# Kernel optimization log

Hardware: AMD Instinct MI355X
Metric: run time of the kernel (lower is better)

## Reference

```python
import jax, jax.numpy as jnp
import numpy as np

N_NODES = 100000
N_EDGES = 1600000
D = 128
N_GRAPHS = 8


def setup_inputs() -> dict:
    key = jax.random.key(0)
    ks = jax.random.split(key, 10)
    x = jax.random.normal(ks[0], (N_NODES, D), dtype=jnp.float32)
    src = jax.random.randint(ks[1], (N_EDGES,), 0, N_NODES)
    dst = jax.random.randint(ks[2], (N_EDGES,), 0, N_NODES)
    graph_ids = jnp.sort(jax.random.randint(ks[3], (N_NODES,), 0, N_GRAPHS))
    s = 1.0 / np.sqrt(D)
    W1 = jax.random.normal(ks[4], (D, D), dtype=jnp.float32) * s
    b1 = jnp.zeros((D,), dtype=jnp.float32)
    W2 = jax.random.normal(ks[5], (D, D), dtype=jnp.float32) * s
    b2 = jnp.zeros((D,), dtype=jnp.float32)
    prelu_a = jnp.full((1,), 0.25, dtype=jnp.float32)
    lin_W = jax.random.normal(ks[6], (D, 1), dtype=jnp.float32) * s
    lin_b = jnp.zeros((1,), dtype=jnp.float32)
    return {"x": x, "src": src, "dst": dst, "graph_ids": graph_ids,
            "W1": W1, "b1": b1, "W2": W2, "b2": b2,
            "prelu_a": prelu_a, "lin_W": lin_W, "lin_b": lin_b}


def _gcn_layer(h, src, dst, n_src, n_dst, W, b):
    # GraphConv with symmetric ('both') normalization: D^{-1/2} A D^{-1/2} H W + b
    h = h @ W                                      # [N, D] small GEMM
    m = h[src] * n_src[:, None]                    # [E, D] gather (irregular)
    agg = jax.ops.segment_sum(m, dst, num_segments=N_NODES)  # scatter-add
    return agg * n_dst[:, None] + b


def reference(x, src, dst, graph_ids, W1, b1, W2, b2, prelu_a, lin_W, lin_b):
    ones_e = jnp.ones((src.shape[0],), dtype=x.dtype)
    deg_out = jnp.maximum(jax.ops.segment_sum(ones_e, src, num_segments=N_NODES), 1.0)
    deg_in = jnp.maximum(jax.ops.segment_sum(ones_e, dst, num_segments=N_NODES), 1.0)
    n_src = jax.lax.rsqrt(deg_out)[src]            # per-edge source norm
    n_dst = jax.lax.rsqrt(deg_in)                  # per-node dest norm

    h = _gcn_layer(x, src, dst, n_src, n_dst, W1, b1)
    h = jax.nn.relu(h)
    h = _gcn_layer(h, src, dst, n_src, n_dst, W2, b2)
    h = jax.nn.relu(h)

    # dgl.mean_nodes: per-graph mean over nodes
    sums = jax.ops.segment_sum(h, graph_ids, num_segments=N_GRAPHS)   # [G, D]
    cnt = jax.ops.segment_sum(jnp.ones((N_NODES,), h.dtype), graph_ids,
                              num_segments=N_GRAPHS)
    pooled = sums / jnp.maximum(cnt, 1.0)[:, None]

    # PReLU (single shared slope) -> Linear -> Sigmoid
    pooled = jnp.where(pooled > 0, pooled, prelu_a[0] * pooled)
    out = jax.nn.sigmoid(pooled @ lin_W + lin_b)   # [G, 1]
    return out
```

## Files before the change

### kernel.cpp

```cpp
#include <hip/hip_runtime.h>
#include <hip/hip_bf16.h>

#define NN 100000
#define NE 1600000
#define DD 128
#define NG 8

#define BSH 8
#define KB 391
#define BMASK 255
#define PB 512
#define CHUNK 3125
#define SCAN_N (KB * PB)

typedef unsigned short u16;
typedef unsigned char u8;
typedef __attribute__((ext_vector_type(8))) short short8;
typedef __attribute__((ext_vector_type(4))) float f32x4;
typedef __attribute__((ext_vector_type(2))) float f32x2;

static __device__ __forceinline__ float bf2f(u16 u) {
  return __uint_as_float(((unsigned)u) << 16);
}
static __device__ __forceinline__ u16 f2bf(float f) {
  unsigned u = __float_as_uint(f);
  u += 0x7fffu + ((u >> 16) & 1);
  return (u16)(u >> 16);
}
static __device__ __forceinline__ u8 f2fp8(float f) {
  return (u8)(__builtin_amdgcn_cvt_pk_fp8_f32(f, f, 0, false) & 0xFF);
}

__global__ void fill_zero(float* __restrict__ p, int n4) {
  int i = blockIdx.x * blockDim.x + threadIdx.x;
  if (i < n4) ((float4*)p)[i] = make_float4(0.f, 0.f, 0.f, 0.f);
}

__global__ void conv_xscale(const float* __restrict__ in, const float* __restrict__ rs_out,
                            u8* __restrict__ out, int n8) {
  int i = blockIdx.x * blockDim.x + threadIdx.x;
  if (i >= n8) return;
  float w = rs_out[i >> 4];
  const float4* p = (const float4*)(in + (size_t)i * 8);
  float4 a = p[0], b = p[1];
  int lo = 0, hi = 0;
  lo = __builtin_amdgcn_cvt_pk_fp8_f32(a.x * w, a.y * w, lo, false);
  lo = __builtin_amdgcn_cvt_pk_fp8_f32(a.z * w, a.w * w, lo, true);
  hi = __builtin_amdgcn_cvt_pk_fp8_f32(b.x * w, b.y * w, hi, false);
  hi = __builtin_amdgcn_cvt_pk_fp8_f32(b.z * w, b.w * w, hi, true);
  ((uint2*)out)[i] = make_uint2((unsigned)lo, (unsigned)hi);
}

__global__ void conv_w_transpose(const float* __restrict__ W, u16* __restrict__ Wt) {
  int idx = blockIdx.x * blockDim.x + threadIdx.x;
  if (idx >= DD * DD) return;
  int n = idx >> 7, k = idx & 127;
  Wt[idx] = f2bf(W[k * DD + n]);
}

__global__ __launch_bounds__(256) void histo_gid(const int* __restrict__ gid,
                                                 int* __restrict__ cnt) {
  __shared__ int h[NG];
  int t = threadIdx.x;
  if (t < NG) h[t] = 0;
  __syncthreads();
  for (int i = blockIdx.x * 256 + t; i < NN; i += gridDim.x * 256)
    atomicAdd(&h[gid[i]], 1);
  __syncthreads();
  if (t < NG && h[t]) atomicAdd(&cnt[t], h[t]);
}

__global__ __launch_bounds__(256) void p1_both(const int* __restrict__ src,
                                               const int* __restrict__ dst,
                                               int* __restrict__ countsS,
                                               int* __restrict__ countsD) {
  __shared__ int hs[KB], hd[KB];
  int t = threadIdx.x, blk = blockIdx.x;
  for (int i = t; i < KB; i += 256) { hs[i] = 0; hd[i] = 0; }
  __syncthreads();
  int e0 = blk * CHUNK;
  for (int i = t; i < CHUNK; i += 256) {
    atomicAdd(&hs[src[e0 + i] >> BSH], 1);
    atomicAdd(&hd[dst[e0 + i] >> BSH], 1);
  }
  __syncthreads();
  for (int i = t; i < KB; i += 256) {
    countsS[i * PB + blk] = hs[i];
    countsD[i * PB + blk] = hd[i];
  }
}

__global__ __launch_bounds__(256) void scanA(int* __restrict__ countsS,
                                             int* __restrict__ countsD,
                                             int* __restrict__ totS,
                                             int* __restrict__ totD) {
  __shared__ int data[PB];
  __shared__ int part[256];
  int b = blockIdx.x;
  int isS = (b < KB);
  int k = isS ? b : b - KB;
  int* counts = isS ? countsS : countsD;
  int* tot = isS ? totS : totD;
  int t = threadIdx.x;
  int* c = counts + (size_t)k * PB;
  data[t] = c[t];
  data[t + 256] = c[t + 256];
  __syncthreads();
  int a0 = data[2 * t], a1 = data[2 * t + 1];
  int s = a0 + a1;
  part[t] = s;
  __syncthreads();
  for (int off = 1; off < 256; off <<= 1) {
    int v = (t >= off) ? part[t - off] : 0;
    __syncthreads();
    part[t] += v;
    __syncthreads();
  }
  int ex = part[t] - s;
  data[2 * t] = ex;
  data[2 * t + 1] = ex + a0;
  __syncthreads();
  c[t] = data[t];
  c[t + 256] = data[t + 256];
  if (t == 255) tot[k] = part[255];
}

__global__ __launch_bounds__(256) void scanB(const int* __restrict__ totS,
                                             const int* __restrict__ totD,
                                             int* __restrict__ baseS,
                                             int* __restrict__ baseD) {
  __shared__ int data[512];
  __shared__ int part[256];
  const int* tot = blockIdx.x ? totD : totS;
  int* base = blockIdx.x ? baseD : baseS;
  int t = threadIdx.x;
  data[t] = (t < KB) ? tot[t] : 0;
  data[t + 256] = (t + 256 < KB) ? tot[t + 256] : 0;
  __syncthreads();
  int a0 = data[2 * t], a1 = data[2 * t + 1];
  int s = a0 + a1;
  part[t] = s;
  __syncthreads();
  for (int off = 1; off < 256; off <<= 1) {
    int v = (t >= off) ? part[t - off] : 0;
    __syncthreads();
    part[t] += v;
    __syncthreads();
  }
  int ex = part[t] - s;
  int i0 = 2 * t, i1 = 2 * t + 1;
  if (i0 <= KB) base[i0] = ex;
  if (i1 <= KB) base[i1] = ex + a0;
}

__global__ __launch_bounds__(256) void p2_both(const int* __restrict__ src,
                                               const int* __restrict__ dst,
                                               const int* __restrict__ countsS,
                                               const int* __restrict__ countsD,
                                               const int* __restrict__ baseS,
                                               const int* __restrict__ baseD,
                                               u8* __restrict__ recsS,
                                               unsigned* __restrict__ recsD) {
  __shared__ int curS[KB], curD[KB];
  int t = threadIdx.x, blk = blockIdx.x;
  for (int i = t; i < KB; i += 256) {
    curS[i] = countsS[i * PB + blk] + baseS[i];
    curD[i] = countsD[i * PB + blk] + baseD[i];
  }
  __syncthreads();
  int e0 = blk * CHUNK;
  for (int i = t; i < CHUNK; i += 256) {
    int s = src[e0 + i];
    int d = dst[e0 + i];
    int ps = atomicAdd(&curS[s >> BSH], 1);
    recsS[ps] = (u8)(s & BMASK);
    int pd = atomicAdd(&curD[d >> BSH], 1);
    recsD[pd] = (unsigned)s | ((unsigned)(d & BMASK) << 17);
  }
}

__global__ __launch_bounds__(256) void src_p3(const u8* __restrict__ recsS,
                                              const int* __restrict__ baseS,
                                              float* __restrict__ rs_out) {
  __shared__ int hist[256];
  int k = blockIdx.x, t = threadIdx.x;
  int rbeg = baseS[k];
  int rend = baseS[k + 1];
  hist[t] = 0;
  __syncthreads();
  for (int i = rbeg + t; i < rend; i += 256) atomicAdd(&hist[recsS[i]], 1);
  __syncthreads();
  int n = (k << BSH) + t;
  if (n < NN) rs_out[n] = rsqrtf(fmaxf((float)hist[t], 1.f));
}

__global__ __launch_bounds__(256) void csr_p3(const unsigned* __restrict__ recs,
                                              const int* __restrict__ baseD,
                                              int* __restrict__ csr_src,
                                              int* __restrict__ cursor_end,
                                              int* __restrict__ deg_in,
                                              float* __restrict__ rs_in) {
  __shared__ int hist[256];
  __shared__ int part[256];
  int k = blockIdx.x, t = threadIdx.x;
  int rbeg = baseD[k];
  int rend = baseD[k + 1];
  hist[t] = 0;
  __syncthreads();
  for (int i = rbeg + t; i < rend; i += 256) atomicAdd(&hist[recs[i] >> 17], 1);
  __syncthreads();
  int h = hist[t];
  part[t] = h;
  __syncthreads();
  for (int off = 1; off < 256; off <<= 1) {
    int v = (t >= off) ? part[t - off] : 0;
    __syncthreads();
    part[t] += v;
    __syncthreads();
  }
  int run = rbeg + part[t] - h;
  int n = (k << BSH) + t;
  if (n < NN) {
    cursor_end[n] = run + h;
    deg_in[n] = h;
    rs_in[n] = rsqrtf(fmaxf((float)h, 1.f));
  }
  hist[t] = run;
  __syncthreads();
  for (int i = rbeg + t; i < rend; i += 256) {
    unsigned r = recs[i];
    int pos = atomicAdd(&hist[r >> 17], 1);
    csr_src[pos] = (int)(r & 0x1FFFF);
  }
}

__global__ __launch_bounds__(256) void gather_agg_fp8(
    const uint4* __restrict__ Hv, const int* __restrict__ csr_src,
    const int* __restrict__ cursor_end, const int* __restrict__ deg_in,
    u16* __restrict__ agg) {
  int node = blockIdx.x * 32 + (threadIdx.x >> 3);
  if (node >= NN) return;
  int q = threadIdx.x & 7;
  int end = cursor_end[node];
  int j = end - deg_in[node];
  float acc[16];
#pragma unroll
  for (int i = 0; i < 16; ++i) acc[i] = 0.f;
#define ACCV(v) { f32x2 t_;                                                        \
  t_ = __builtin_amdgcn_cvt_pk_f32_fp8((int)(v).x, false); acc[0] += t_.x;  acc[1] += t_.y;  \
  t_ = __builtin_amdgcn_cvt_pk_f32_fp8((int)(v).x, true);  acc[2] += t_.x;  acc[3] += t_.y;  \
  t_ = __builtin_amdgcn_cvt_pk_f32_fp8((int)(v).y, false); acc[4] += t_.x;  acc[5] += t_.y;  \
  t_ = __builtin_amdgcn_cvt_pk_f32_fp8((int)(v).y, true);  acc[6] += t_.x;  acc[7] += t_.y;  \
  t_ = __builtin_amdgcn_cvt_pk_f32_fp8((int)(v).z, false); acc[8] += t_.x;  acc[9] += t_.y;  \
  t_ = __builtin_amdgcn_cvt_pk_f32_fp8((int)(v).z, true);  acc[10] += t_.x; acc[11] += t_.y; \
  t_ = __builtin_amdgcn_cvt_pk_f32_fp8((int)(v).w, false); acc[12] += t_.x; acc[13] += t_.y; \
  t_ = __builtin_amdgcn_cvt_pk_f32_fp8((int)(v).w, true);  acc[14] += t_.x; acc[15] += t_.y; }
  for (; j + 4 <= end; j += 4) {
    int s0 = csr_src[j + 0];
    int s1 = csr_src[j + 1];
    int s2 = csr_src[j + 2];
    int s3 = csr_src[j + 3];
    uint4 v0 = Hv[(size_t)s0 * 8 + q];
    uint4 v1 = Hv[(size_t)s1 * 8 + q];
    uint4 v2 = Hv[(size_t)s2 * 8 + q];
    uint4 v3 = Hv[(size_t)s3 * 8 + q];
    ACCV(v0) ACCV(v1) ACCV(v2) ACCV(v3)
  }
  for (; j < end; ++j) {
    uint4 v = Hv[(size_t)csr_src[j] * 8 + q];
    ACCV(v)
  }
#undef ACCV
  uint4 o0, o1;
  o0.x = (unsigned)f2bf(acc[0])  | ((unsigned)f2bf(acc[1])  << 16);
  o0.y = (unsigned)f2bf(acc[2])  | ((unsigned)f2bf(acc[3])  << 16);
  o0.z = (unsigned)f2bf(acc[4])  | ((unsigned)f2bf(acc[5])  << 16);
  o0.w = (unsigned)f2bf(acc[6])  | ((unsigned)f2bf(acc[7])  << 16);
  o1.x = (unsigned)f2bf(acc[8])  | ((unsigned)f2bf(acc[9])  << 16);
  o1.y = (unsigned)f2bf(acc[10]) | ((unsigned)f2bf(acc[11]) << 16);
  o1.z = (unsigned)f2bf(acc[12]) | ((unsigned)f2bf(acc[13]) << 16);
  o1.w = (unsigned)f2bf(acc[14]) | ((unsigned)f2bf(acc[15]) << 16);
  u16* op = agg + (size_t)node * DD + q * 16;
  *(uint4*)op = o0;
  *(uint4*)(op + 8) = o1;
}

#define GEMM_PRE                                                              \
  __shared__ uint4 Wl4[2048];                                      \
  int tid = threadIdx.x;                                                      \
  {                                                                           \
    const uint4* Wg4 = (const uint4*)Wt;                                      \
    for (int i = tid; i < 2048; i += 256) {                                   \
      int row = i >> 4, c = i & 15;                                           \
      Wl4[(row << 4) | (c ^ (row & 15))] = Wg4[i];                            \
    }                                                                         \
  }                                                                           \
  int wid = tid >> 6;                                                         \
  int lane = tid & 63;                                                        \
  int l15 = lane & 15;                                                        \
  int kg = lane >> 4;                                                         \
  int rowbase = blockIdx.x * 128 + wid * 32;                                  \
  f32x4 acc[2][8];                                                            \
  short8 a[2][4];                                                             \
  _Pragma("unroll")                                                           \
  for (int t = 0; t < 2; ++t) {                                               \
    int arow = rowbase + t * 16 + l15;                                        \
    bool ok = arow < NN;                                                      \
    const u16* aptr = Ab + (size_t)arow * DD + kg * 8;                        \
    _Pragma("unroll")                                                         \
    for (int kt = 0; kt < 4; ++kt) {                                          \
      a[t][kt] = ok ? *(const short8*)(aptr + kt * 32)                        \
                    : (short8){0, 0, 0, 0, 0, 0, 0, 0};                       \
      acc[0][kt] = (f32x4){0.f, 0.f, 0.f, 0.f};                               \
      acc[0][kt + 4] = (f32x4){0.f, 0.f, 0.f, 0.f};                           \
      acc[1][kt] = (f32x4){0.f, 0.f, 0.f, 0.f};                               \
      acc[1][kt + 4] = (f32x4){0.f, 0.f, 0.f, 0.f};                           \
    }                                                                         \
  }                                                                           \
  __syncthreads();                                                            \
  _Pragma("unroll")                                                           \
  for (int n = 0; n < 8; ++n) {                                               \
    _Pragma("unroll")                                                         \
    for (int kt = 0; kt < 4; ++kt) {                                          \
      short8 b = *(const short8*)(Wl4 + (((n * 16 + l15) << 4) |              \
                                         ((kg + kt * 4) ^ l15)));             \
      acc[0][n] = __builtin_amdgcn_mfma_f32_16x16x32_bf16(a[0][kt], b, acc[0][n], 0, 0, 0); \
      acc[1][n] = __builtin_amdgcn_mfma_f32_16x16x32_bf16(a[1][kt], b, acc[1][n], 0, 0, 0); \
    }                                                                         \
  }

__global__ __launch_bounds__(256) void gemm_mfma_fp8out(
    const u16* __restrict__ Ab, const u16* __restrict__ Wt,
    const float* __restrict__ bias, const float* __restrict__ rs,
    const float* __restrict__ post, u8* __restrict__ Cb) {
  GEMM_PRE
#pragma unroll
  for (int t = 0; t < 2; ++t) {
    int crow0 = rowbase + t * 16 + kg * 4;
#pragma unroll
    for (int j = 0; j < 4; ++j) {
      int r = crow0 + j;
      if (r < NN) {
        float s = rs[r];
        float ps = post[r];
#pragma unroll
        for (int n = 0; n < 8; ++n) {
          float v = fmaxf(acc[t][n][j] * s + bias[n * 16 + l15], 0.f) * ps;
          Cb[(size_t)r * DD + n * 16 + l15] = f2fp8(v);
        }
      }
    }
  }
}

__global__ __launch_bounds__(256) void gemm_mfma_pool(
    const u16* __restrict__ Ab, const u16* __restrict__ Wt,
    const float* __restrict__ bias, const float* __restrict__ rs,
    const int* __restrict__ gid, float* __restrict__ pooled) {
  __shared__ float pl[NG * DD];
  for (int i = threadIdx.x; i < NG * DD; i += 256) pl[i] = 0.f;
  GEMM_PRE
  float pacc[8];
#pragma unroll
  for (int n = 0; n < 8; ++n) pacc[n] = 0.f;
  int curg = -1;
#pragma unroll
  for (int t = 0; t < 2; ++t) {
    int crow0 = rowbase + t * 16 + kg * 4;
#pragma unroll
    for (int j = 0; j < 4; ++j) {
      int r = crow0 + j;
      if (r < NN) {
        int g = gid[r];
        if (g != curg) {
          if (curg >= 0) {
#pragma unroll
            for (int n = 0; n < 8; ++n) {
              atomicAdd(&pl[curg * DD + n * 16 + l15], pacc[n]);
              pacc[n] = 0.f;
            }
          }
          curg = g;
        }
        float s = rs[r];
#pragma unroll
        for (int n = 0; n < 8; ++n)
          pacc[n] += fmaxf(acc[t][n][j] * s + bias[n * 16 + l15], 0.f);
      }
    }
  }
  if (curg >= 0) {
#pragma unroll
    for (int n = 0; n < 8; ++n)
      atomicAdd(&pl[curg * DD + n * 16 + l15], pacc[n]);
  }
  __syncthreads();
  int rlo = blockIdx.x * 128;
  int rhi = rlo + 127;
  if (rhi >= NN) rhi = NN - 1;
  int gmin = gid[rlo];
  int gmax = gid[rhi];
  int span = (gmax - gmin + 1) * DD;
  for (int i = tid; i < span; i += 256) {
    float v = pl[gmin * DD + i];
    if (v != 0.f) atomicAdd(&pooled[gmin * DD + i], v);
  }
}

__global__ __launch_bounds__(128) void final_kernel(const float* __restrict__ pooled,
                                                    const int* __restrict__ cnt,
                                                    const float* __restrict__ prelu_a,
                                                    const float* __restrict__ linW,
                                                    const float* __restrict__ linb,
                                                    float* __restrict__ out) {
  int t = threadIdx.x;
  __shared__ float red[2];
  float w = linW[t];
  float alpha = prelu_a[0];
  float lb = linb[0];
  for (int g = 0; g < NG; ++g) {
    float v = pooled[g * DD + t] / fmaxf((float)cnt[g], 1.f);
    v = v > 0.f ? v : alpha * v;
    float p = v * w;
#pragma unroll
    for (int off = 32; off >= 1; off >>= 1) p += __shfl_down(p, off, 64);
    if ((t & 63) == 0) red[t >> 6] = p;
    __syncthreads();
    if (t == 0) {
      float s = red[0] + red[1] + lb;
      out[g] = 1.f / (1.f + expf(-s));
    }
    __syncthreads();
  }
}

extern "C" void kernel_launch(void* const* d_in, const int* in_sizes, int n_in,
                              void* d_out, int out_size, void* d_ws, size_t ws_size,
                              hipStream_t stream) {
  const float* x   = (const float*)d_in[0];
  const int*   src = (const int*)d_in[1];
  const int*   dst = (const int*)d_in[2];
  const int*   gid = (const int*)d_in[3];
  const float* W1  = (const float*)d_in[4];
  const float* b1  = (const float*)d_in[5];
  const float* W2  = (const float*)d_in[6];
  const float* b2  = (const float*)d_in[7];
  const float* pa  = (const float*)d_in[8];
  const float* lW  = (const float*)d_in[9];
  const float* lb  = (const float*)d_in[10];
  float* out = (float*)d_out;

  char* ws = (char*)d_ws;
  size_t o = 0;
  auto alloc = [&](size_t bytes) {
    size_t r = o;
    o += (bytes + 255) & ~(size_t)255;
    return r;
  };
  int*   deg_in  = (int*)(ws + alloc((size_t)NN * 4));
  float* rs_out  = (float*)(ws + alloc((size_t)NN * 4));
  float* rs_in   = (float*)(ws + alloc((size_t)NN * 4));
  int*   countsS = (int*)(ws + alloc((size_t)SCAN_N * 4));
  int*   countsD = (int*)(ws + alloc((size_t)SCAN_N * 4));
  int*   totS    = (int*)(ws + alloc((size_t)KB * 4));
  int*   totD    = (int*)(ws + alloc((size_t)KB * 4));
  int*   baseS   = (int*)(ws + alloc((size_t)(KB + 1) * 4));
  int*   baseD   = (int*)(ws + alloc((size_t)(KB + 1) * 4));
  int*   cursor_end = (int*)(ws + alloc((size_t)NN * 4));
  u8*    recsS   = (u8*)(ws + alloc((size_t)NE));
  unsigned* recsD = (unsigned*)(ws + alloc((size_t)NE * 4));
  int*   csr_src = (int*)(ws + alloc((size_t)NE * 4));
  u16*   Wt1     = (u16*)(ws + alloc((size_t)DD * DD * 2));
  u16*   Wt2     = (u16*)(ws + alloc((size_t)DD * DD * 2));
  u8*    bufA    = (u8*)(ws + alloc((size_t)NN * DD));
  u8*    bufB    = (u8*)(ws + alloc((size_t)NN * DD));
  u16*   aggbuf  = (u16*)(ws + alloc((size_t)NN * DD * 2));
  float* pooled  = (float*)(ws + alloc((size_t)(NG * DD + NG) * 4));
  int*   cnt     = (int*)(pooled + NG * DD);

  fill_zero<<<2, 256, 0, stream>>>(pooled, (NG * DD + NG + 3) / 4);
  histo_gid<<<98, 256, 0, stream>>>(gid, cnt);

  p1_both<<<PB, 256, 0, stream>>>(src, dst, countsS, countsD);
  scanA<<<2 * KB, 256, 0, stream>>>(countsS, countsD, totS, totD);
  scanB<<<2, 256, 0, stream>>>(totS, totD, baseS, baseD);
  p2_both<<<PB, 256, 0, stream>>>(src, dst, countsS, countsD, baseS, baseD, recsS, recsD);
  src_p3<<<KB, 256, 0, stream>>>(recsS, baseS, rs_out);
  csr_p3<<<KB, 256, 0, stream>>>(recsD, baseD, csr_src, cursor_end, deg_in, rs_in);

  conv_xscale<<<(NN * DD / 8 + 255) / 256, 256, 0, stream>>>(x, rs_out, bufA, NN * DD / 8);
  conv_w_transpose<<<64, 256, 0, stream>>>(W1, Wt1);
  conv_w_transpose<<<64, 256, 0, stream>>>(W2, Wt2);

  const int gablocks = (NN + 31) / 32;
  const int gmblocks = (NN + 127) / 128;

  gather_agg_fp8<<<gablocks, 256, 0, stream>>>((const uint4*)bufA, csr_src, cursor_end, deg_in, aggbuf);
  gemm_mfma_fp8out<<<gmblocks, 256, 0, stream>>>(aggbuf, Wt1, b1, rs_in, rs_out, bufB);

  gather_agg_fp8<<<gablocks, 256, 0, stream>>>((const uint4*)bufB, csr_src, cursor_end, deg_in, aggbuf);
  gemm_mfma_pool<<<gmblocks, 256, 0, stream>>>(aggbuf, Wt2, b2, rs_in, gid, pooled);

  final_kernel<<<1, 128, 0, stream>>>(pooled, cnt, pa, lW, lb, out);
}
```

Measured before the change: 212.3 us.

## Slice fp8 features into column-major slices for gather, fuse preprocessing kernels

Stores the fp8 node features as 8 slices of 16 bytes per node, so each gather block handles one slice for 256 nodes. Each slice (1.6 MB) is small enough to stay cached during the random gathers. It also merges the W transposes, graph-id histogram and pooled zeroing into the first histogram kernel, and merges the source and destination degree/CSR passes into one launch, which cuts launch count. The trade-off is that each edge index is now read eight times (once per slice) and each thread loads one 16-byte value per edge instead of eight lanes sharing a 128-byte row.

```diff
diff --git a/kernel.cpp b/kernel.cpp
--- a/kernel.cpp
+++ b/kernel.cpp
@@ -12,6 +12,8 @@
 #define PB 512
 #define CHUNK 3125
 #define SCAN_N (KB * PB)
+#define NSL 8
+#define GHB 98
 
 typedef unsigned short u16;
 typedef unsigned char u8;
@@ -31,16 +33,12 @@
   return (u8)(__builtin_amdgcn_cvt_pk_fp8_f32(f, f, 0, false) & 0xFF);
 }
 
-__global__ void fill_zero(float* __restrict__ p, int n4) {
-  int i = blockIdx.x * blockDim.x + threadIdx.x;
-  if (i < n4) ((float4*)p)[i] = make_float4(0.f, 0.f, 0.f, 0.f);
-}
-
 __global__ void conv_xscale(const float* __restrict__ in, const float* __restrict__ rs_out,
                             u8* __restrict__ out, int n8) {
   int i = blockIdx.x * blockDim.x + threadIdx.x;
   if (i >= n8) return;
-  float w = rs_out[i >> 4];
+  int node = i >> 4, c = i & 15;
+  float w = rs_out[node];
   const float4* p = (const float4*)(in + (size_t)i * 8);
   float4 a = p[0], b = p[1];
   int lo = 0, hi = 0;
@@ -48,45 +46,57 @@
   lo = __builtin_amdgcn_cvt_pk_fp8_f32(a.z * w, a.w * w, lo, true);
   hi = __builtin_amdgcn_cvt_pk_fp8_f32(b.x * w, b.y * w, hi, false);
   hi = __builtin_amdgcn_cvt_pk_fp8_f32(b.z * w, b.w * w, hi, true);
-  ((uint2*)out)[i] = make_uint2((unsigned)lo, (unsigned)hi);
-}
-
-__global__ void conv_w_transpose(const float* __restrict__ W, u16* __restrict__ Wt) {
-  int idx = blockIdx.x * blockDim.x + threadIdx.x;
-  if (idx >= DD * DD) return;
-  int n = idx >> 7, k = idx & 127;
-  Wt[idx] = f2bf(W[k * DD + n]);
-}
-
-__global__ __launch_bounds__(256) void histo_gid(const int* __restrict__ gid,
-                                                 int* __restrict__ cnt) {
-  __shared__ int h[NG];
-  int t = threadIdx.x;
-  if (t < NG) h[t] = 0;
-  __syncthreads();
-  for (int i = blockIdx.x * 256 + t; i < NN; i += gridDim.x * 256)
-    atomicAdd(&h[gid[i]], 1);
-  __syncthreads();
-  if (t < NG && h[t]) atomicAdd(&cnt[t], h[t]);
-}
-
-__global__ __launch_bounds__(256) void p1_both(const int* __restrict__ src,
-                                               const int* __restrict__ dst,
-                                               int* __restrict__ countsS,
-                                               int* __restrict__ countsD) {
+  *(uint2*)(out + ((size_t)(c >> 1) * NN + node) * 16 + (c & 1) * 8) =
+      make_uint2((unsigned)lo, (unsigned)hi);
+}
+
+__global__ __launch_bounds__(256) void p1x(const int* __restrict__ src,
+                                           const int* __restrict__ dst,
+                                           int* __restrict__ countsS,
+                                           int* __restrict__ countsD,
+                                           const float* __restrict__ W1,
+                                           const float* __restrict__ W2,
+                                           u16* __restrict__ Wt1,
+                                           u16* __restrict__ Wt2,
+                                           const int* __restrict__ gid,
+                                           int* __restrict__ cnt_part,
+                                           float* __restrict__ pooled) {
   __shared__ int hs[KB], hd[KB];
-  int t = threadIdx.x, blk = blockIdx.x;
-  for (int i = t; i < KB; i += 256) { hs[i] = 0; hd[i] = 0; }
-  __syncthreads();
-  int e0 = blk * CHUNK;
-  for (int i = t; i < CHUNK; i += 256) {
-    atomicAdd(&hs[src[e0 + i] >> BSH], 1);
-    atomicAdd(&hd[dst[e0 + i] >> BSH], 1);
-  }
-  __syncthreads();
-  for (int i = t; i < KB; i += 256) {
-    countsS[i * PB + blk] = hs[i];
-    countsD[i * PB + blk] = hd[i];
+  __shared__ int h8[NG];
+  int t = threadIdx.x, b = blockIdx.x;
+  if (b < PB) {
+    for (int i = t; i < KB; i += 256) { hs[i] = 0; hd[i] = 0; }
+    __syncthreads();
+    int e0 = b * CHUNK;
+    for (int i = t; i < CHUNK; i += 256) {
+      atomicAdd(&hs[src[e0 + i] >> BSH], 1);
+      atomicAdd(&hd[dst[e0 + i] >> BSH], 1);
+    }
+    __syncthreads();
+    for (int i = t; i < KB; i += 256) {
+      countsS[i * PB + b] = hs[i];
+      countsD[i * PB + b] = hd[i];
+    }
+  } else if (b < PB + 128) {
+    int i = (b - PB) * 256 + t;
+    if (i < DD * DD) {
+      int n = i >> 7, k = i & 127;
+      Wt1[i] = f2bf(W1[k * DD + n]);
+    } else {
+      int i2 = i - DD * DD;
+      int n = i2 >> 7, k = i2 & 127;
+      Wt2[i2] = f2bf(W2[k * DD + n]);
+    }
+  } else if (b < PB + 128 + GHB) {
+    int blk = b - PB - 128;
+    if (t < NG) h8[t] = 0;
+    __syncthreads();
+    for (int i = blk * 256 + t; i < NN; i += GHB * 256)
+      atomicAdd(&h8[gid[i]], 1);
+    __syncthreads();
+    if (t < NG) cnt_part[blk * NG + t] = h8[t];
+  } else {
+    for (int i = t; i < NG * DD; i += 256) pooled[i] = 0.f;
   }
 }
 
@@ -179,68 +189,70 @@
   }
 }
 
-__global__ __launch_bounds__(256) void src_p3(const u8* __restrict__ recsS,
-                                              const int* __restrict__ baseS,
-                                              float* __restrict__ rs_out) {
-  __shared__ int hist[256];
-  int k = blockIdx.x, t = threadIdx.x;
-  int rbeg = baseS[k];
-  int rend = baseS[k + 1];
-  hist[t] = 0;
-  __syncthreads();
-  for (int i = rbeg + t; i < rend; i += 256) atomicAdd(&hist[recsS[i]], 1);
-  __syncthreads();
-  int n = (k << BSH) + t;
-  if (n < NN) rs_out[n] = rsqrtf(fmaxf((float)hist[t], 1.f));
-}
-
-__global__ __launch_bounds__(256) void csr_p3(const unsigned* __restrict__ recs,
-                                              const int* __restrict__ baseD,
-                                              int* __restrict__ csr_src,
-                                              int* __restrict__ cursor_end,
-                                              int* __restrict__ deg_in,
-                                              float* __restrict__ rs_in) {
+__global__ __launch_bounds__(256) void sd_p3(const u8* __restrict__ recsS,
+                                             const int* __restrict__ baseS,
+                                             float* __restrict__ rs_out,
+                                             const unsigned* __restrict__ recsD,
+                                             const int* __restrict__ baseD,
+                                             int* __restrict__ csr_src,
+                                             int* __restrict__ cursor_end,
+                                             int* __restrict__ deg_in,
+                                             float* __restrict__ rs_in) {
   __shared__ int hist[256];
   __shared__ int part[256];
-  int k = blockIdx.x, t = threadIdx.x;
-  int rbeg = baseD[k];
-  int rend = baseD[k + 1];
-  hist[t] = 0;
-  __syncthreads();
-  for (int i = rbeg + t; i < rend; i += 256) atomicAdd(&hist[recs[i] >> 17], 1);
-  __syncthreads();
-  int h = hist[t];
-  part[t] = h;
-  __syncthreads();
-  for (int off = 1; off < 256; off <<= 1) {
-    int v = (t >= off) ? part[t - off] : 0;
-    __syncthreads();
-    part[t] += v;
-    __syncthreads();
-  }
-  int run = rbeg + part[t] - h;
-  int n = (k << BSH) + t;
-  if (n < NN) {
-    cursor_end[n] = run + h;
-    deg_in[n] = h;
-    rs_in[n] = rsqrtf(fmaxf((float)h, 1.f));
-  }
-  hist[t] = run;
-  __syncthreads();
-  for (int i = rbeg + t; i < rend; i += 256) {
-    unsigned r = recs[i];
-    int pos = atomicAdd(&hist[r >> 17], 1);
-    csr_src[pos] = (int)(r & 0x1FFFF);
-  }
-}
-
-__global__ __launch_bounds__(256) void gather_agg_fp8(
-    const uint4* __restrict__ Hv, const int* __restrict__ csr_src,
+  int t = threadIdx.x;
+  if (blockIdx.x < KB) {
+    int k = blockIdx.x;
+    int rbeg = baseS[k];
+    int rend = baseS[k + 1];
+    hist[t] = 0;
+    __syncthreads();
+    for (int i = rbeg + t; i < rend; i += 256) atomicAdd(&hist[recsS[i]], 1);
+    __syncthreads();
+    int n = (k << BSH) + t;
+    if (n < NN) rs_out[n] = rsqrtf(fmaxf((float)hist[t], 1.f));
+  } else {
+    int k = blockIdx.x - KB;
+    int rbeg = baseD[k];
+    int rend = baseD[k + 1];
+    hist[t] = 0;
+    __syncthreads();
+    for (int i = rbeg + t; i < rend; i += 256) atomicAdd(&hist[recsD[i] >> 17], 1);
+    __syncthreads();
+    int h = hist[t];
+    part[t] = h;
+    __syncthreads();
+    for (int off = 1; off < 256; off <<= 1) {
+      int v = (t >= off) ? part[t - off] : 0;
+      __syncthreads();
+      part[t] += v;
+      __syncthreads();
+    }
+    int run = rbeg + part[t] - h;
+    int n = (k << BSH) + t;
+    if (n < NN) {
+      cursor_end[n] = run + h;
+      deg_in[n] = h;
+      rs_in[n] = rsqrtf(fmaxf((float)h, 1.f));
+    }
+    hist[t] = run;
+    __syncthreads();
+    for (int i = rbeg + t; i < rend; i += 256) {
+      unsigned r = recsD[i];
+      int pos = atomicAdd(&hist[r >> 17], 1);
+      csr_src[pos] = (int)(r & 0x1FFFF);
+    }
+  }
+}
+
+__global__ __launch_bounds__(256) void gather_slice(
+    const uint4* __restrict__ Hs, const int* __restrict__ csr_src,
     const int* __restrict__ cursor_end, const int* __restrict__ deg_in,
     u16* __restrict__ agg) {
-  int node = blockIdx.x * 32 + (threadIdx.x >> 3);
+  int slice = blockIdx.x & (NSL - 1);
+  int node = (blockIdx.x >> 3) * 256 + threadIdx.x;
   if (node >= NN) return;
-  int q = threadIdx.x & 7;
+  const uint4* H = Hs + (size_t)slice * NN;
   int end = cursor_end[node];
   int j = end - deg_in[node];
   float acc[16];
@@ -260,14 +272,14 @@
     int s1 = csr_src[j + 1];
     int s2 = csr_src[j + 2];
     int s3 = csr_src[j + 3];
-    uint4 v0 = Hv[(size_t)s0 * 8 + q];
-    uint4 v1 = Hv[(size_t)s1 * 8 + q];
-    uint4 v2 = Hv[(size_t)s2 * 8 + q];
-    uint4 v3 = Hv[(size_t)s3 * 8 + q];
+    uint4 v0 = H[s0];
+    uint4 v1 = H[s1];
+    uint4 v2 = H[s2];
+    uint4 v3 = H[s3];
     ACCV(v0) ACCV(v1) ACCV(v2) ACCV(v3)
   }
   for (; j < end; ++j) {
-    uint4 v = Hv[(size_t)csr_src[j] * 8 + q];
+    uint4 v = H[csr_src[j]];
     ACCV(v)
   }
 #undef ACCV
@@ -280,7 +292,7 @@
   o1.y = (unsigned)f2bf(acc[10]) | ((unsigned)f2bf(acc[11]) << 16);
   o1.z = (unsigned)f2bf(acc[12]) | ((unsigned)f2bf(acc[13]) << 16);
   o1.w = (unsigned)f2bf(acc[14]) | ((unsigned)f2bf(acc[15]) << 16);
-  u16* op = agg + (size_t)node * DD + q * 16;
+  u16* op = agg + (size_t)node * DD + slice * 16;
   *(uint4*)op = o0;
   *(uint4*)(op + 8) = o1;
 }
@@ -346,7 +358,7 @@
 #pragma unroll
         for (int n = 0; n < 8; ++n) {
           float v = fmaxf(acc[t][n][j] * s + bias[n * 16 + l15], 0.f) * ps;
-          Cb[(size_t)r * DD + n * 16 + l15] = f2fp8(v);
+          Cb[((size_t)n * NN + r) * 16 + l15] = f2fp8(v);
         }
       }
     }
@@ -408,18 +420,25 @@
 }
 
 __global__ __launch_bounds__(128) void final_kernel(const float* __restrict__ pooled,
-                                                    const int* __restrict__ cnt,
+                                                    const int* __restrict__ cnt_part,
                                                     const float* __restrict__ prelu_a,
                                                     const float* __restrict__ linW,
                                                     const float* __restrict__ linb,
                                                     float* __restrict__ out) {
   int t = threadIdx.x;
   __shared__ float red[2];
+  __shared__ int cntl[NG];
+  if (t < NG) {
+    int s = 0;
+    for (int b = 0; b < GHB; ++b) s += cnt_part[b * NG + t];
+    cntl[t] = s;
+  }
+  __syncthreads();
   float w = linW[t];
   float alpha = prelu_a[0];
   float lb = linb[0];
   for (int g = 0; g < NG; ++g) {
-    float v = pooled[g * DD + t] / fmaxf((float)cnt[g], 1.f);
+    float v = pooled[g * DD + t] / fmaxf((float)cntl[g], 1.f);
     v = v > 0.f ? v : alpha * v;
     float p = v * w;
 #pragma unroll
@@ -475,31 +494,24 @@
   u8*    bufA    = (u8*)(ws + alloc((size_t)NN * DD));
   u8*    bufB    = (u8*)(ws + alloc((size_t)NN * DD));
   u16*   aggbuf  = (u16*)(ws + alloc((size_t)NN * DD * 2));
-  float* pooled  = (float*)(ws + alloc((size_t)(NG * DD + NG) * 4));
-  int*   cnt     = (int*)(pooled + NG * DD);
-
-  fill_zero<<<2, 256, 0, stream>>>(pooled, (NG * DD + NG + 3) / 4);
-  histo_gid<<<98, 256, 0, stream>>>(gid, cnt);
-
-  p1_both<<<PB, 256, 0, stream>>>(src, dst, countsS, countsD);
+  float* pooled  = (float*)(ws + alloc((size_t)NG * DD * 4));
+  int*   cnt_part = (int*)(ws + alloc((size_t)GHB * NG * 4));
+
+  p1x<<<PB + 128 + GHB + 1, 256, 0, stream>>>(src, dst, countsS, countsD,
+                                              W1, W2, Wt1, Wt2, gid, cnt_part, pooled);
   scanA<<<2 * KB, 256, 0, stream>>>(countsS, countsD, totS, totD);
   scanB<<<2, 256, 0, stream>>>(totS, totD, baseS, baseD);
   p2_both<<<PB, 256, 0, stream>>>(src, dst, countsS, countsD, baseS, baseD, recsS, recsD);
-  src_p3<<<KB, 256, 0, stream>>>(recsS, baseS, rs_out);
-  csr_p3<<<KB, 256, 0, stream>>>(recsD, baseD, csr_src, cursor_end, deg_in, rs_in);
-
+  sd_p3<<<2 * KB, 256, 0, stream>>>(recsS, baseS, rs_out,
+                                    recsD, baseD, csr_src, cursor_end, deg_in, rs_in);
   conv_xscale<<<(NN * DD / 8 + 255) / 256, 256, 0, stream>>>(x, rs_out, bufA, NN * DD / 8);
-  conv_w_transpose<<<64, 256, 0, stream>>>(W1, Wt1);
-  conv_w_transpose<<<64, 256, 0, stream>>>(W2, Wt2);
-
-  const int gablocks = (NN + 31) / 32;
+
+  const int gablocks = KB * NSL;
   const int gmblocks = (NN + 127) / 128;
 
-  gather_agg_fp8<<<gablocks, 256, 0, stream>>>((const uint4*)bufA, csr_src, cursor_end, deg_in, aggbuf);
+  gather_slice<<<gablocks, 256, 0, stream>>>((const uint4*)bufA, csr_src, cursor_end, deg_in, aggbuf);
   gemm_mfma_fp8out<<<gmblocks, 256, 0, stream>>>(aggbuf, Wt1, b1, rs_in, rs_out, bufB);
-
-  gather_agg_fp8<<<gablocks, 256, 0, stream>>>((const uint4*)bufB, csr_src, cursor_end, deg_in, aggbuf);
+  gather_slice<<<gablocks, 256, 0, stream>>>((const uint4*)bufB, csr_src, cursor_end, deg_in, aggbuf);
   gemm_mfma_pool<<<gmblocks, 256, 0, stream>>>(aggbuf, Wt2, b2, rs_in, gid, pooled);
-
-  final_kernel<<<1, 128, 0, stream>>>(pooled, cnt, pa, lW, lb, out);
-}
+  final_kernel<<<1, 128, 0, stream>>>(pooled, cnt_part, pa, lW, lb, out);
+}
```

Result: slower. 283.3 us (+33.4%).
